# Optimization experiments

Measured on AMD Instinct MI355X. Metric: run time of the kernel, lower is better.

The kernel has to match this reference:

```python
import jax, jax.numpy as jnp
import numpy as np

PSA_TYPE = 0  # 0 = 'collect', 1 = 'distribute'
H_MASK = 97
W_MASK = 97


def psamask(x, psa_type, h_mask, w_mask):
    """Faithful JAX port of mmcv PSAMask.
    collect:    out[b, nh*W+nw, h, w] = x[b, (nh-h+hh)*wm + (nw-w+hw), h, w]
    distribute: out[b, h*W+w, nh, nw] = x[b, (nh-h+hh)*wm + (nw-w+hw), h, w]
    where hh=(h_mask-1)//2, hw=(w_mask-1)//2 and entries outside the local
    mask window are zero.
    """
    B, C, H, W = x.shape
    half_h = (h_mask - 1) // 2
    half_w = (w_mask - 1) // 2
    h = jnp.arange(H)
    w = jnp.arange(W)
    # hidx[nh, h] = mask row index for neighbor nh of pixel row h
    hidx = h[:, None] - h[None, :] + half_h          # (H, H)
    widx = w[:, None] - w[None, :] + half_w          # (W, W)
    vh = (hidx >= 0) & (hidx < h_mask)
    vw = (widx >= 0) & (widx < w_mask)
    hc = jnp.clip(hidx, 0, h_mask - 1).astype(jnp.int32)
    wc = jnp.clip(widx, 0, w_mask - 1).astype(jnp.int32)
    if psa_type == 0:
        # output layout (nh, nw, h, w)
        cidx = hc[:, None, :, None] * w_mask + wc[None, :, None, :]   # (H, W, H, W)
        valid = vh[:, None, :, None] & vw[None, :, None, :]
        out = x[:, cidx, h[None, None, :, None], w[None, None, None, :]]  # (B, H, W, H, W)
    else:
        # output layout (h, w, nh, nw)
        cidx = hc.T[:, None, :, None] * w_mask + wc.T[None, :, None, :]
        valid = vh.T[:, None, :, None] & vw.T[None, :, None, :]
        out = x[:, cidx, h[:, None, None, None], w[None, :, None, None]]
    out = jnp.where(valid[None], out, 0.0)
    return out.reshape(B, H * W, H, W)


def setup_inputs() -> dict:
    key = jax.random.key(0)
    B, H, W = 1, 97, 97
    x = jax.random.normal(key, (B, H_MASK * W_MASK, H, W), dtype=jnp.float32)
    return {"x": x}


def reference(x):
    return psamask(x, PSA_TYPE, H_MASK, W_MASK)
```

## Files before the change

kernel.cpp:

```cpp
#include <hip/hip_runtime.h>


#define HW97   97
#define PLANE  9409
#define HALF   48
#define LDSTR  98
#define NTHREADS 256

__global__ __launch_bounds__(NTHREADS)
void psamask_collect_kernel(const float* __restrict__ x, float* __restrict__ out) {
    const int h  = blockIdx.x;
    const int nh = blockIdx.y;
    const int a  = nh - h + HALF;
    const unsigned tid = threadIdx.x;

    float* __restrict__ outp = out + (size_t)(nh * HW97) * PLANE + h * HW97;

    if (a < 0 || a >= HW97) {
        for (unsigned idx = tid; idx < PLANE; idx += NTHREADS) {
            unsigned nw = idx / HW97;
            unsigned w  = idx - nw * HW97;
            outp[(size_t)nw * PLANE + w] = 0.0f;
        }
        return;
    }

    __shared__ float lds[HW97 * LDSTR];

    const float* __restrict__ xp = x + (size_t)(a * HW97) * PLANE + h * HW97;
    for (unsigned idx = tid; idx < PLANE; idx += NTHREADS) {
        unsigned b = idx / HW97;
        unsigned w = idx - b * HW97;
        lds[b * LDSTR + w] = xp[(size_t)b * PLANE + w];
    }
    __syncthreads();

    for (unsigned idx = tid; idx < PLANE; idx += NTHREADS) {
        unsigned nw = idx / HW97;
        unsigned w  = idx - nw * HW97;
        int b = (int)nw - (int)w + HALF;
        float v = (b >= 0 && b < HW97) ? lds[b * LDSTR + w] : 0.0f;
        outp[(size_t)nw * PLANE + w] = v;
    }
}

extern "C" void kernel_launch(void* const* d_in, const int* in_sizes, int n_in,
                              void* d_out, int out_size, void* d_ws, size_t ws_size,
                              hipStream_t stream) {
    const float* x = (const float*)d_in[0];
    float* out = (float*)d_out;
    dim3 grid(HW97, HW97);
    psamask_collect_kernel<<<grid, NTHREADS, 0, stream>>>(x, out);
}
```

Baseline: 185.3 us.

## Use direct global-to-LDS loads with skewed layout and incremental index math

```diff
diff --git a/kernel.cpp b/kernel.cpp
--- a/kernel.cpp
+++ b/kernel.cpp
@@ -1,46 +1,85 @@
 #include <hip/hip_runtime.h>
 
 
-#define HW97   97
-#define PLANE  9409
-#define HALF   48
-#define LDSTR  98
-#define NTHREADS 256
+#define HW    97
+#define PLANE 9409
+#define HALF  48
+#define NT    512
+#define NITER 19
 
-__global__ __launch_bounds__(NTHREADS)
+typedef const __attribute__((address_space(1))) void* gptr_t;
+typedef __attribute__((address_space(3))) void* lptr_t;
+
+__global__ __launch_bounds__(NT)
 void psamask_collect_kernel(const float* __restrict__ x, float* __restrict__ out) {
     const int h  = blockIdx.x;
     const int nh = blockIdx.y;
     const int a  = nh - h + HALF;
     const unsigned tid = threadIdx.x;
 
-    float* __restrict__ outp = out + (size_t)(nh * HW97) * PLANE + h * HW97;
+    float* __restrict__ outp = out + (size_t)(nh * HW) * PLANE + h * HW;
 
-    if (a < 0 || a >= HW97) {
-        for (unsigned idx = tid; idx < PLANE; idx += NTHREADS) {
-            unsigned nw = idx / HW97;
-            unsigned w  = idx - nw * HW97;
-            outp[(size_t)nw * PLANE + w] = 0.0f;
+    const unsigned r0 = tid / HW;
+    const unsigned c0 = tid - r0 * HW;
+
+    if ((unsigned)a >= HW) {
+        unsigned w   = c0;
+        unsigned off = r0 * PLANE + c0;
+        #pragma unroll
+        for (int k = 0; k < NITER; ++k) {
+            unsigned d = tid + (unsigned)k * NT;
+            if (d < PLANE) outp[off] = 0.0f;
+            w += 27;
+            bool wrap = (w >= HW);
+            off += wrap ? (6u * PLANE - 70u) : (5u * PLANE + 27u);
+            if (wrap) w -= HW;
         }
         return;
     }
 
-    __shared__ float lds[HW97 * LDSTR];
+    __shared__ float lds[PLANE];
 
-    const float* __restrict__ xp = x + (size_t)(a * HW97) * PLANE + h * HW97;
-    for (unsigned idx = tid; idx < PLANE; idx += NTHREADS) {
-        unsigned b = idx / HW97;
-        unsigned w = idx - b * HW97;
-        lds[b * LDSTR + w] = xp[(size_t)b * PLANE + w];
+    const float* __restrict__ xp = x + (size_t)(a * HW) * PLANE + h * HW;
+    {
+        unsigned b = r0, cw = c0;
+        #pragma unroll
+        for (int k = 0; k < NITER; ++k) {
+            unsigned d = tid + (unsigned)k * NT;
+            if (d < PLANE) {
+                unsigned w = cw - b + ((cw < b) ? HW : 0u);
+                const float* g = xp + b * PLANE + w;
+                unsigned d0 = (unsigned)k * NT + (tid & ~63u);
+                __builtin_amdgcn_global_load_lds((gptr_t)g, (lptr_t)&lds[d0], 4, 0, 0);
+            }
+            b += 5; cw += 27;
+            if (cw >= HW) { cw -= HW; b += 1; }
+        }
     }
+    asm volatile("s_waitcnt vmcnt(0)" ::: "memory");
     __syncthreads();
 
-    for (unsigned idx = tid; idx < PLANE; idx += NTHREADS) {
-        unsigned nw = idx / HW97;
-        unsigned w  = idx - nw * HW97;
-        int b = (int)nw - (int)w + HALF;
-        float v = (b >= 0 && b < HW97) ? lds[b * LDSTR + w] : 0.0f;
-        outp[(size_t)nw * PLANE + w] = v;
+    {
+        unsigned w   = c0;
+        int      b   = (int)r0 - (int)c0 + HALF;
+        unsigned cw  = r0 + HALF; if (cw >= HW) cw -= HW;
+        unsigned off = r0 * PLANE + c0;
+        #pragma unroll
+        for (int k = 0; k < NITER; ++k) {
+            unsigned d = tid + (unsigned)k * NT;
+            if (d < PLANE) {
+                bool valid = ((unsigned)b < HW);
+                unsigned bc = valid ? (unsigned)b : 0u;
+                float v = lds[bc * HW + cw];
+                outp[off] = valid ? v : 0.0f;
+            }
+            w += 27;
+            bool wrap = (w >= HW);
+            if (wrap) w -= HW;
+            b  += wrap ? 76 : -22;
+            cw += wrap ? 6u : 5u;
+            if (cw >= HW) cw -= HW;
+            off += wrap ? (6u * PLANE - 70u) : (5u * PLANE + 27u);
+        }
     }
 }
 
@@ -49,6 +88,6 @@
                               hipStream_t stream) {
     const float* x = (const float*)d_in[0];
     float* out = (float*)d_out;
-    dim3 grid(HW97, HW97);
-    psamask_collect_kernel<<<grid, NTHREADS, 0, stream>>>(x, out);
+    dim3 grid(HW, HW);
+    psamask_collect_kernel<<<grid, NT, 0, stream>>>(x, out);
 }
```

After: 184.2 us. About the same (-0.6%).

## Persistent double-buffered kernel with async global-to-LDS loads and XCD-aware scheduling

Applied to the files above, without the earlier changes.

```diff
diff --git a/kernel.cpp b/kernel.cpp
--- a/kernel.cpp
+++ b/kernel.cpp
@@ -1,46 +1,123 @@
 #include <hip/hip_runtime.h>
 
 
-#define HW97   97
-#define PLANE  9409
-#define HALF   48
-#define LDSTR  98
-#define NTHREADS 256
+#define HW    97
+#define PLANE 9409
+#define HALF  48
+#define NT    1024
+#define SSTR  9536
+#define ZOFF  9472
+#define LNK   10
+#define SNK   19
+#define TOT2  18818
 
-__global__ __launch_bounds__(NTHREADS)
-void psamask_collect_kernel(const float* __restrict__ x, float* __restrict__ out) {
-    const int h  = blockIdx.x;
-    const int nh = blockIdx.y;
-    const int a  = nh - h + HALF;
+typedef const __attribute__((address_space(1))) void* gptr_t;
+typedef __attribute__((address_space(3))) void* lptr_t;
+
+__global__ __launch_bounds__(NT)
+void psamask_persistent(const float* __restrict__ x, float* __restrict__ out) {
     const unsigned tid = threadIdx.x;
+    const unsigned xcd = blockIdx.x & 7u;
+    const unsigned j   = blockIdx.x >> 3;
+    const unsigned cnt = (xcd == 0u) ? 13u : 12u;
+    const unsigned T   = cnt * 49u;
+    const unsigned s0  = (j * T) >> 6;
+    const unsigned s1  = ((j + 1u) * T) >> 6;
+    const int n = (int)(s1 - s0);
 
-    float* __restrict__ outp = out + (size_t)(nh * HW97) * PLANE + h * HW97;
+    __shared__ float lds[4 * SSTR];
 
-    if (a < 0 || a >= HW97) {
-        for (unsigned idx = tid; idx < PLANE; idx += NTHREADS) {
-            unsigned nw = idx / HW97;
-            unsigned w  = idx - nw * HW97;
-            outp[(size_t)nw * PLANE + w] = 0.0f;
-        }
-        return;
+    unsigned loff[LNK], ldst[LNK];
+    #pragma unroll
+    for (int k = 0; k < LNK; ++k) {
+        unsigned d = tid + (unsigned)k * NT; if (d > PLANE - 1u) d = PLANE - 1u;
+        unsigned b = d / HW, cw = d - b * HW;
+        unsigned ws = cw - b + ((cw < b) ? HW : 0u);
+        loff[k] = b * PLANE + ws;
+        unsigned dd = (unsigned)k * NT + (tid & ~63u);
+        ldst[k] = (dd > 9408u) ? 9408u : dd;
+    }
+    unsigned soff[SNK], srd[SNK], shp[SNK];
+    #pragma unroll
+    for (int k = 0; k < SNK; ++k) {
+        unsigned d = tid + (unsigned)k * NT; if (d > TOT2 - 1u) d = TOT2 - 1u;
+        unsigned q = d / 194u, e = d - q * 194u;
+        unsigned hp = (e >= HW) ? 1u : 0u;
+        unsigned w  = e - hp * HW;
+        int bb = (int)q - (int)w + HALF;
+        bool vb = ((unsigned)bb < HW);
+        unsigned bc = vb ? (unsigned)bb : 0u;
+        unsigned cw = q + HALF; if (cw >= HW) cw -= HW;
+        soff[k] = q * PLANE + e;
+        srd[k]  = vb ? (hp * SSTR + bc * HW + cw) : (hp * SSTR + ZOFF);
+        shp[k]  = hp;
     }
 
-    __shared__ float lds[HW97 * LDSTR];
+    if (tid < 4u) lds[tid * SSTR + ZOFF] = 0.0f;
 
-    const float* __restrict__ xp = x + (size_t)(a * HW97) * PLANE + h * HW97;
-    for (unsigned idx = tid; idx < PLANE; idx += NTHREADS) {
-        unsigned b = idx / HW97;
-        unsigned w = idx - b * HW97;
-        lds[b * LDSTR + w] = xp[(size_t)b * PLANE + w];
+    auto stage = [&](int a0, int h0, unsigned bufsel) {
+        #pragma unroll
+        for (int p = 0; p < 2; ++p) {
+            int a = a0 - p;
+            unsigned ac = (a < 0) ? 0u : ((a > 96) ? 96u : (unsigned)a);
+            const float* xp = x + (size_t)(ac * HW) * PLANE + (unsigned)(h0 + p) * HW;
+            unsigned dbase = bufsel * (2u * SSTR) + (unsigned)p * SSTR;
+            #pragma unroll
+            for (int k = 0; k < LNK; ++k)
+                __builtin_amdgcn_global_load_lds((gptr_t)(xp + loff[k]),
+                                                 (lptr_t)&lds[dbase + ldst[k]], 4, 0, 0);
+        }
+    };
+
+    auto wr = [&](int a0, int h0, int nh, unsigned bufsel) {
+        float* op = out + (size_t)((unsigned)nh * HW) * PLANE + (unsigned)h0 * HW;
+        const bool av0 = ((unsigned)a0 < HW);
+        const bool av1 = ((unsigned)(a0 - 1) < HW);
+        const unsigned bbase = bufsel * (2u * SSTR);
+        if (av0 && av1) {
+            #pragma unroll
+            for (int k = 0; k < SNK; ++k)
+                op[soff[k]] = lds[bbase + srd[k]];
+        } else if (!av0 && !av1) {
+            #pragma unroll
+            for (int k = 0; k < SNK; ++k)
+                op[soff[k]] = 0.0f;
+        } else {
+            #pragma unroll
+            for (int k = 0; k < SNK; ++k) {
+                float v = lds[bbase + srd[k]];
+                bool av = shp[k] ? av1 : av0;
+                op[soff[k]] = av ? v : 0.0f;
+            }
+        }
+    };
+
+    unsigned g = s0 / 49u, cc = s0 - g * 49u;
+    {
+        int nh = (int)(8u * g + xcd);
+        int h0 = 2 * (int)cc; if (h0 > 95) h0 = 95;
+        stage(nh - h0 + HALF, h0, 0u);
     }
-    __syncthreads();
+    asm volatile("s_waitcnt vmcnt(0) lgkmcnt(0)" ::: "memory");
+    __builtin_amdgcn_s_barrier();
 
-    for (unsigned idx = tid; idx < PLANE; idx += NTHREADS) {
-        unsigned nw = idx / HW97;
-        unsigned w  = idx - nw * HW97;
-        int b = (int)nw - (int)w + HALF;
-        float v = (b >= 0 && b < HW97) ? lds[b * LDSTR + w] : 0.0f;
-        outp[(size_t)nw * PLANE + w] = v;
+    for (int i = 0; i < n; ++i) {
+        int nh = (int)(8u * g + xcd);
+        int h0 = 2 * (int)cc; if (h0 > 95) h0 = 95;
+        int a0 = nh - h0 + HALF;
+
+        unsigned gn = g, cn = cc + 1u;
+        if (cn == 49u) { cn = 0u; gn += 1u; }
+        if (i + 1 < n) {
+            int nh2 = (int)(8u * gn + xcd);
+            int h02 = 2 * (int)cn; if (h02 > 95) h02 = 95;
+            stage(nh2 - h02 + HALF, h02, (unsigned)((i + 1) & 1));
+        }
+        wr(a0, h0, nh, (unsigned)(i & 1));
+
+        asm volatile("s_waitcnt vmcnt(19) lgkmcnt(0)" ::: "memory");
+        __builtin_amdgcn_s_barrier();
+        g = gn; cc = cn;
     }
 }
 
@@ -49,6 +126,5 @@
                               hipStream_t stream) {
     const float* x = (const float*)d_in[0];
     float* out = (float*)d_out;
-    dim3 grid(HW97, HW97);
-    psamask_collect_kernel<<<grid, NTHREADS, 0, stream>>>(x, out);
+    psamask_persistent<<<dim3(512), NT, 0, stream>>>(x, out);
 }
```

Measured after the change: 187.6 us. About the same (+1.3%).

## Gather sheared rows into LDS via global_load_lds, then write contiguous float4 rows

Applied to the files above, without the earlier changes.

```diff
diff --git a/kernel.cpp b/kernel.cpp
--- a/kernel.cpp
+++ b/kernel.cpp
@@ -1,46 +1,98 @@
 #include <hip/hip_runtime.h>
 
 
-#define HW97   97
-#define PLANE  9409
-#define HALF   48
-#define LDSTR  98
-#define NTHREADS 256
+#define HW    97
+#define PLANE 9409
+#define HALF  48
+#define NT    512
+#define RSTR  196
+#define NLDS  19456
+#define DITER 38
+#define NV4   4656
+#define V4IT  10
 
-__global__ __launch_bounds__(NTHREADS)
-void psamask_collect_kernel(const float* __restrict__ x, float* __restrict__ out) {
-    const int h  = blockIdx.x;
-    const int nh = blockIdx.y;
-    const int a  = nh - h + HALF;
+typedef const __attribute__((address_space(1))) void* gptr_t;
+typedef __attribute__((address_space(3))) void* lptr_t;
+using f4v = __attribute__((ext_vector_type(4))) float;
+typedef f4v f4v_u __attribute__((aligned(4)));
+
+__device__ const float g_zero[16] = {};
+
+__global__ __launch_bounds__(NT)
+void psamask_shear(const float* __restrict__ x, float* __restrict__ out) {
+    const unsigned l   = blockIdx.x;
+    const unsigned xcd = l & 7u;
+    const unsigned m   = l >> 3;
+    const unsigned g   = m / 49u;
+    const unsigned cc  = m - g * 49u;
+    const int nh = (int)(g * 8u + xcd);
+    if (nh > 96) return;
+
+    int h0 = 2 * (int)cc; if (h0 > 95) h0 = 95;
     const unsigned tid = threadIdx.x;
 
-    float* __restrict__ outp = out + (size_t)(nh * HW97) * PLANE + h * HW97;
+    __shared__ float lds[NLDS];
 
-    if (a < 0 || a >= HW97) {
-        for (unsigned idx = tid; idx < PLANE; idx += NTHREADS) {
-            unsigned nw = idx / HW97;
-            unsigned w  = idx - nw * HW97;
-            outp[(size_t)nw * PLANE + w] = 0.0f;
+    const int a0  = nh - h0 + HALF;
+    const unsigned av0 = ((unsigned)a0       < HW) ? 1u : 0u;
+    const unsigned av1 = ((unsigned)(a0 - 1) < HW) ? 1u : 0u;
+
+    const unsigned ac0 = (a0 < 0) ? 0u : ((a0 > 96) ? 96u : (unsigned)a0);
+    const int a1 = a0 - 1;
+    const unsigned ac1 = (a1 < 0) ? 0u : ((a1 > 96) ? 96u : (unsigned)a1);
+    const float* __restrict__ xb0 =
+        x + (size_t)(ac0 * HW) * PLANE + (unsigned)h0 * HW;
+    const float* __restrict__ xb1 =
+        x + (size_t)(ac1 * HW) * PLANE + (unsigned)(h0 + 1) * HW;
+    const float* zp = &g_zero[tid & 15u];
+
+    {
+        unsigned q = tid / RSTR;
+        unsigned e = tid - q * RSTR;
+        #pragma unroll
+        for (int k = 0; k < DITER; ++k) {
+            unsigned pad = (e >= 194u) | (q >= 97u);
+            unsigned p   = (e >= HW && e < 194u) ? 1u : 0u;
+            unsigned w   = e - p * HW;
+            int b = (int)q - (int)w + HALF;
+            unsigned vb = ((unsigned)b < HW) ? 1u : 0u;
+            unsigned pv = p ? av1 : av0;
+            bool use = (vb & pv & (1u - pad)) != 0u;
+            const float* base = p ? xb1 : xb0;
+            const float* src  = use ? (base + (unsigned)b * PLANE + w) : zp;
+            unsigned d0 = (unsigned)k * NT + (tid & ~63u);
+            __builtin_amdgcn_global_load_lds((gptr_t)src, (lptr_t)&lds[d0], 4, 0, 0);
+            e += 120u; q += 2u;
+            if (e >= RSTR) { e -= RSTR; q += 1u; }
         }
-        return;
     }
-
-    __shared__ float lds[HW97 * LDSTR];
-
-    const float* __restrict__ xp = x + (size_t)(a * HW97) * PLANE + h * HW97;
-    for (unsigned idx = tid; idx < PLANE; idx += NTHREADS) {
-        unsigned b = idx / HW97;
-        unsigned w = idx - b * HW97;
-        lds[b * LDSTR + w] = xp[(size_t)b * PLANE + w];
-    }
+    asm volatile("s_waitcnt vmcnt(0)" ::: "memory");
     __syncthreads();
 
-    for (unsigned idx = tid; idx < PLANE; idx += NTHREADS) {
-        unsigned nw = idx / HW97;
-        unsigned w  = idx - nw * HW97;
-        int b = (int)nw - (int)w + HALF;
-        float v = (b >= 0 && b < HW97) ? lds[b * LDSTR + w] : 0.0f;
-        outp[(size_t)nw * PLANE + w] = v;
+    float* __restrict__ outp =
+        out + (size_t)((unsigned)nh * HW) * PLANE + (unsigned)h0 * HW;
+    {
+        unsigned q = tid / 48u;
+        unsigned i = tid - q * 48u;
+        unsigned loff = q * RSTR + 4u * i;
+        unsigned goff = q * PLANE + 4u * i;
+        #pragma unroll
+        for (int k = 0; k < V4IT; ++k) {
+            unsigned v = tid + (unsigned)k * NT;
+            if (v < NV4) {
+                f4v val = *(const f4v*)&lds[loff];
+                *(f4v_u*)(outp + goff) = val;
+            }
+            i += 32u; loff += 10u * RSTR + 128u; goff += 10u * PLANE + 128u;
+            if (i >= 48u) { i -= 48u; loff += RSTR - 192u; goff += PLANE - 192u; }
+            q += 10u;
+        }
+    }
+    if (tid < HW) {
+        unsigned lo = tid * RSTR + 192u;
+        unsigned go = tid * PLANE + 192u;
+        outp[go]      = lds[lo];
+        outp[go + 1u] = lds[lo + 1u];
     }
 }
 
@@ -49,6 +101,5 @@
                               hipStream_t stream) {
     const float* x = (const float*)d_in[0];
     float* out = (float*)d_out;
-    dim3 grid(HW97, HW97);
-    psamask_collect_kernel<<<grid, NTHREADS, 0, stream>>>(x, out);
+    psamask_shear<<<dim3(5096), NT, 0, stream>>>(x, out);
 }
```

Result: slower. 282.2 us (+52.3%).
